# Kernel tuning notes

Hardware: AMD Instinct MI355X
Metric: run time of the kernel (lower is better)

## Reference

```python
import jax, jax.numpy as jnp
import numpy as np

TEMPERATURE = 0.1


def setup_inputs() -> dict:
    key = jax.random.key(0)
    k1, k2 = jax.random.split(key)
    N, D = 4096, 128
    return {
        "anchor_embeddings": jax.random.normal(k1, (N, D), dtype=jnp.float32),
        "target_embeddings": jax.random.normal(k2, (N, D), dtype=jnp.float32),
    }


def _l2_normalize(x, axis=-1, eps=1e-12):
    # matches tf.math.l2_normalize
    sq = jnp.sum(x * x, axis=axis, keepdims=True)
    return x * jax.lax.rsqrt(jnp.maximum(sq, eps))


def reference(anchor_embeddings, target_embeddings):
    N = anchor_embeddings.shape[0]
    # l2-normalize both views; cosine_similarity of unit vectors == dot product,
    # so the original's broadcasted (2N,2N,D) product + internal re-normalization
    # reduces to a single [2N,D] @ [D,2N] matmul.
    a = _l2_normalize(anchor_embeddings, axis=1)
    t = _l2_normalize(target_embeddings, axis=1)
    z = jnp.concatenate([a, t], axis=0)              # [2N, D]
    sim = jnp.einsum("id,jd->ij", z, z)              # [2N, 2N]

    # positives: diag_part(k=+N) and diag_part(k=-N)
    sim_ij = jnp.diagonal(sim, offset=N)             # [N]
    sim_ji = jnp.diagonal(sim, offset=-N)            # [N]
    positives = jnp.concatenate([sim_ij, sim_ji], axis=0)  # [2N]

    logits = sim / TEMPERATURE                       # [2N, 2N]
    # negative_mask = ~eye(2N): exclude self-similarity from the denominator
    diag_mask = jnp.eye(2 * N, dtype=bool)
    denom = jnp.sum(jnp.where(diag_mask, 0.0, jnp.exp(logits)), axis=1)  # [2N]

    loss_partial = -(positives / TEMPERATURE - jnp.log(denom))           # [2N]
    loss = jnp.sum(loss_partial) / (2 * N)
    return loss
```

## Files before the change

kernel.cpp:

```cpp
#include <hip/hip_runtime.h>

#define N_ROWS 4096
#define TN 8192
#define DIM 128
#define SQRT_C 3.79828266f

#define Z_BYTE_OFF 36864

typedef __attribute__((ext_vector_type(8))) short short8;
typedef __attribute__((ext_vector_type(4))) float f32x4;

static __device__ __forceinline__ ushort f2bf(float f) {
    union { float f; unsigned u; } a; a.f = f;
    unsigned r = a.u + 0x7FFF + ((a.u >> 16) & 1);
    return (ushort)(r >> 16);
}

__global__ __launch_bounds__(256) void prep_kernel(
    const float* __restrict__ anchor, const float* __restrict__ target,
    ushort* __restrict__ z, float* __restrict__ pos_part)
{
    int wave = threadIdx.x >> 6;
    int lane = threadIdx.x & 63;
    int i    = blockIdx.x * 4 + wave;
    float2 a = ((const float2*)(anchor + (size_t)i * DIM))[lane];
    float2 t = ((const float2*)(target + (size_t)i * DIM))[lane];
    float sa = a.x * a.x + a.y * a.y;
    float st = t.x * t.x + t.y * t.y;
    float dt = a.x * t.x + a.y * t.y;
    #pragma unroll
    for (int m = 1; m < 64; m <<= 1) {
        sa += __shfl_xor(sa, m, 64);
        st += __shfl_xor(st, m, 64);
        dt += __shfl_xor(dt, m, 64);
    }
    float rsa = rsqrtf(fmaxf(sa, 1e-12f));
    float rst = rsqrtf(fmaxf(st, 1e-12f));
    float ka = rsa * SQRT_C, kt = rst * SQRT_C;
    ushort2 za, zt;
    za.x = f2bf(a.x * ka); za.y = f2bf(a.y * ka);
    zt.x = f2bf(t.x * kt); zt.y = f2bf(t.y * kt);
    ((ushort2*)(z + (size_t)i * DIM))[lane] = za;
    ((ushort2*)(z + (size_t)(i + N_ROWS) * DIM))[lane] = zt;
    __shared__ float red[4];
    if (lane == 0) red[wave] = dt * rsa * rst;
    __syncthreads();
    if (threadIdx.x == 0)
        pos_part[blockIdx.x] = red[0] + red[1] + red[2] + red[3];
}

__global__ __launch_bounds__(256) void simgemm_kernel(
    const ushort* __restrict__ z, float* __restrict__ denom)
{
    int wave = threadIdx.x >> 6;
    int lane = threadIdx.x & 63;
    int r = lane & 15;
    int g = lane >> 4;
    int wr = wave >> 1, wc = wave & 1;
    int rowbase = blockIdx.x * 128 + wr * 64;
    int wcol    = blockIdx.y * 512 + wc * 256;

    short8 a[4][4];
    #pragma unroll
    for (int rt = 0; rt < 4; ++rt)
        #pragma unroll
        for (int kt = 0; kt < 4; ++kt)
            a[rt][kt] = *(const short8*)(z + (size_t)(rowbase + rt * 16 + r) * DIM
                                           + kt * 32 + g * 8);

    float ps[4][4];
    #pragma unroll
    for (int rt = 0; rt < 4; ++rt)
        #pragma unroll
        for (int q = 0; q < 4; ++q) ps[rt][q] = 0.0f;

    bool wavediag = ((unsigned)(rowbase - wcol) < 256u);

    const ushort* pb = z + (size_t)(wcol + r) * DIM + g * 8;

#define LOADB(buf, ptr)                                \
    {   buf[0] = *(const short8*)(ptr);                \
        buf[1] = *(const short8*)((ptr) + 32);         \
        buf[2] = *(const short8*)((ptr) + 64);         \
        buf[3] = *(const short8*)((ptr) + 96); }

#define COMPUTE(ct, b)                                                        \
    {   int c0 = wcol + (ct) * 16;                                            \
        bool dtile = wavediag && ((unsigned)(c0 - rowbase) < 64u);            \
        if (!dtile) {                                                         \
            _Pragma("unroll")                                                 \
            for (int rt = 0; rt < 4; ++rt) {                                  \
                f32x4 acc = {0.f, 0.f, 0.f, 0.f};                             \
                _Pragma("unroll")                                             \
                for (int kt = 0; kt < 4; ++kt)                                \
                    acc = __builtin_amdgcn_mfma_f32_16x16x32_bf16(            \
                        a[rt][kt], b[kt], acc, 0, 0, 0);                      \
                _Pragma("unroll")                                             \
                for (int q = 0; q < 4; ++q)                                   \
                    ps[rt][q] += __builtin_amdgcn_exp2f(acc[q]);              \
            }                                                                 \
        } else {                                                              \
            int gcol = c0 + r;                                                \
            _Pragma("unroll")                                                 \
            for (int rt = 0; rt < 4; ++rt) {                                  \
                f32x4 acc = {0.f, 0.f, 0.f, 0.f};                             \
                _Pragma("unroll")                                             \
                for (int kt = 0; kt < 4; ++kt)                                \
                    acc = __builtin_amdgcn_mfma_f32_16x16x32_bf16(            \
                        a[rt][kt], b[kt], acc, 0, 0, 0);                      \
                _Pragma("unroll")                                             \
                for (int q = 0; q < 4; ++q) {                                 \
                    float e = __builtin_amdgcn_exp2f(acc[q]);                 \
                    int grow = rowbase + rt * 16 + g * 4 + q;                 \
                    ps[rt][q] += (grow == gcol) ? 0.0f : e;                   \
                }                                                             \
            }                                                                 \
        } }

    short8 b0[4], b1[4];
    LOADB(b0, pb);
    for (int ct = 0; ct < 16; ct += 2) {
        const ushort* pn = pb + (ct + 1) * (16 * DIM);
        LOADB(b1, pn);
        COMPUTE(ct, b0);
        if (ct + 2 < 16) {
            const ushort* pn2 = pb + (ct + 2) * (16 * DIM);
            LOADB(b0, pn2);
        }
        COMPUTE(ct + 1, b1);
    }
#undef LOADB
#undef COMPUTE

    #pragma unroll
    for (int rt = 0; rt < 4; ++rt)
        #pragma unroll
        for (int q = 0; q < 4; ++q) {
            float v = ps[rt][q];
            v += __shfl_xor(v, 1, 64);
            v += __shfl_xor(v, 2, 64);
            v += __shfl_xor(v, 4, 64);
            v += __shfl_xor(v, 8, 64);
            if (r == 0)
                atomicAdd(&denom[rowbase + rt * 16 + g * 4 + q], v);
        }
}

__global__ __launch_bounds__(1024) void finalize_kernel(
    const float* __restrict__ denom, const float* __restrict__ pos_part,
    float* __restrict__ out)
{
    int tid = threadIdx.x;
    float slog = 0.0f;
    #pragma unroll
    for (int u = 0; u < TN / 1024; ++u) slog += logf(denom[u * 1024 + tid]);
    float spos = pos_part[tid];
    #pragma unroll
    for (int m = 1; m < 64; m <<= 1) {
        slog += __shfl_xor(slog, m, 64);
        spos += __shfl_xor(spos, m, 64);
    }
    __shared__ float redl[16], redp[16];
    if ((tid & 63) == 0) { redl[tid >> 6] = slog; redp[tid >> 6] = spos; }
    __syncthreads();
    if (tid == 0) {
        float tl = 0.0f, tp = 0.0f;
        #pragma unroll
        for (int i = 0; i < 16; ++i) { tl += redl[i]; tp += redp[i]; }
        out[0] = (tl - 20.0f * tp) / (float)TN;
    }
}

extern "C" void kernel_launch(void* const* d_in, const int* in_sizes, int n_in,
                              void* d_out, int out_size, void* d_ws, size_t ws_size,
                              hipStream_t stream) {
    const float* anchor = (const float*)d_in[0];
    const float* target = (const float*)d_in[1];
    float* denom    = (float*)d_ws;
    float* pos_part = denom + TN;
    ushort* z       = (ushort*)((char*)d_ws + Z_BYTE_OFF);

    hipMemsetAsync(d_ws, 0, TN * sizeof(float), stream);
    prep_kernel<<<N_ROWS / 4, 256, 0, stream>>>(anchor, target, z, pos_part);
    simgemm_kernel<<<dim3(TN / 128, 16), 256, 0, stream>>>(z, denom);
    finalize_kernel<<<1, 1024, 0, stream>>>(denom, pos_part, (float*)d_out);
}
```

Measured before the change: 104.0 us.

## Fuse memset and finalize into neighbouring kernels, retile GEMM with deeper prefetch

The host memset is dropped: prep_kernel now zeroes the denom buffer and the ticket itself. The separate finalize kernel is removed, and the last GEMM block to finish (found through an atomic ticket) computes the final loss. The GEMM tiling is reshaped to 64 rows by 1024 columns per block, and each wave now holds 2 A row tiles, walks 32 column tiles, prefetches three tiles ahead and asks for 2 blocks per CU. This cuts launch overhead and register pressure, at the cost of fewer A rows reused per B load and a serial tail reduction inside a single block.

```diff
diff --git a/kernel.cpp b/kernel.cpp
--- a/kernel.cpp
+++ b/kernel.cpp
@@ -5,7 +5,8 @@
 #define DIM 128
 #define SQRT_C 3.79828266f
 
-#define Z_BYTE_OFF 36864
+#define Z_BYTE_OFF 40960
+#define NBLOCKS_GEMM 1024
 
 typedef __attribute__((ext_vector_type(8))) short short8;
 typedef __attribute__((ext_vector_type(4))) float f32x4;
@@ -18,8 +19,12 @@
 
 __global__ __launch_bounds__(256) void prep_kernel(
     const float* __restrict__ anchor, const float* __restrict__ target,
-    ushort* __restrict__ z, float* __restrict__ pos_part)
+    ushort* __restrict__ z, float* __restrict__ pos_part,
+    float* __restrict__ denom, unsigned* __restrict__ ticket)
 {
+    if (threadIdx.x < 8) denom[blockIdx.x * 8 + threadIdx.x] = 0.0f;
+    if (blockIdx.x == 0 && threadIdx.x == 8) *ticket = 0u;
+
     int wave = threadIdx.x >> 6;
     int lane = threadIdx.x & 63;
     int i    = blockIdx.x * 4 + wave;
@@ -49,47 +54,51 @@
         pos_part[blockIdx.x] = red[0] + red[1] + red[2] + red[3];
 }
 
-__global__ __launch_bounds__(256) void simgemm_kernel(
-    const ushort* __restrict__ z, float* __restrict__ denom)
+__global__ __launch_bounds__(256, 2) void simgemm_kernel(
+    const ushort* __restrict__ z, float* __restrict__ denom,
+    const float* __restrict__ pos_part, unsigned* __restrict__ ticket,
+    float* __restrict__ out)
 {
     int wave = threadIdx.x >> 6;
     int lane = threadIdx.x & 63;
     int r = lane & 15;
     int g = lane >> 4;
     int wr = wave >> 1, wc = wave & 1;
-    int rowbase = blockIdx.x * 128 + wr * 64;
-    int wcol    = blockIdx.y * 512 + wc * 256;
-
-    short8 a[4][4];
-    #pragma unroll
-    for (int rt = 0; rt < 4; ++rt)
-        #pragma unroll
-        for (int kt = 0; kt < 4; ++kt)
+    int rowbase = blockIdx.x * 64 + wr * 32;
+    int wcol    = blockIdx.y * 1024 + wc * 512;
+
+    short8 a[2][4];
+    #pragma unroll
+    for (int rt = 0; rt < 2; ++rt)
+        #pragma unroll
+        for (int kt = 0; kt < 4; ++kt) {
             a[rt][kt] = *(const short8*)(z + (size_t)(rowbase + rt * 16 + r) * DIM
                                            + kt * 32 + g * 8);
-
-    float ps[4][4];
-    #pragma unroll
-    for (int rt = 0; rt < 4; ++rt)
+            asm volatile("" : "+v"(*(f32x4*)&a[rt][kt]));
+        }
+
+    float ps[2][4];
+    #pragma unroll
+    for (int rt = 0; rt < 2; ++rt)
         #pragma unroll
         for (int q = 0; q < 4; ++q) ps[rt][q] = 0.0f;
 
-    bool wavediag = ((unsigned)(rowbase - wcol) < 256u);
-
+    bool wavediag = ((unsigned)(rowbase - wcol) < 512u);
     const ushort* pb = z + (size_t)(wcol + r) * DIM + g * 8;
 
-#define LOADB(buf, ptr)                                \
-    {   buf[0] = *(const short8*)(ptr);                \
-        buf[1] = *(const short8*)((ptr) + 32);         \
-        buf[2] = *(const short8*)((ptr) + 64);         \
-        buf[3] = *(const short8*)((ptr) + 96); }
-
-#define COMPUTE(ct, b)                                                        \
-    {   int c0 = wcol + (ct) * 16;                                            \
-        bool dtile = wavediag && ((unsigned)(c0 - rowbase) < 64u);            \
+#define LOADB(buf, t)                                                  \
+    {   const ushort* p_ = pb + (size_t)(t) * (16 * DIM);              \
+        buf[0] = *(const short8*)(p_);                                 \
+        buf[1] = *(const short8*)(p_ + 32);                            \
+        buf[2] = *(const short8*)(p_ + 64);                            \
+        buf[3] = *(const short8*)(p_ + 96); }
+
+#define COMPUTE(t, b)                                                         \
+    {   int c0 = wcol + (t) * 16;                                             \
+        bool dtile = wavediag && ((unsigned)(c0 - rowbase) < 32u);            \
         if (!dtile) {                                                         \
             _Pragma("unroll")                                                 \
-            for (int rt = 0; rt < 4; ++rt) {                                  \
+            for (int rt = 0; rt < 2; ++rt) {                                  \
                 f32x4 acc = {0.f, 0.f, 0.f, 0.f};                             \
                 _Pragma("unroll")                                             \
                 for (int kt = 0; kt < 4; ++kt)                                \
@@ -102,7 +111,7 @@
         } else {                                                              \
             int gcol = c0 + r;                                                \
             _Pragma("unroll")                                                 \
-            for (int rt = 0; rt < 4; ++rt) {                                  \
+            for (int rt = 0; rt < 2; ++rt) {                                  \
                 f32x4 acc = {0.f, 0.f, 0.f, 0.f};                             \
                 _Pragma("unroll")                                             \
                 for (int kt = 0; kt < 4; ++kt)                                \
@@ -117,23 +126,24 @@
             }                                                                 \
         } }
 
-    short8 b0[4], b1[4];
-    LOADB(b0, pb);
-    for (int ct = 0; ct < 16; ct += 2) {
-        const ushort* pn = pb + (ct + 1) * (16 * DIM);
-        LOADB(b1, pn);
-        COMPUTE(ct, b0);
-        if (ct + 2 < 16) {
-            const ushort* pn2 = pb + (ct + 2) * (16 * DIM);
-            LOADB(b0, pn2);
-        }
-        COMPUTE(ct + 1, b1);
+    short8 b0[4], b1[4], b2[4], b3[4];
+    LOADB(b0, 0); LOADB(b1, 1); LOADB(b2, 2);
+    #pragma unroll
+    for (int t = 0; t < 32; t += 4) {
+        LOADB(b3, t + 3);
+        COMPUTE(t, b0);
+        LOADB(b0, (t + 4 <= 31 ? t + 4 : 31));
+        COMPUTE(t + 1, b1);
+        LOADB(b1, (t + 5 <= 31 ? t + 5 : 31));
+        COMPUTE(t + 2, b2);
+        LOADB(b2, (t + 6 <= 31 ? t + 6 : 31));
+        COMPUTE(t + 3, b3);
     }
 #undef LOADB
 #undef COMPUTE
 
     #pragma unroll
-    for (int rt = 0; rt < 4; ++rt)
+    for (int rt = 0; rt < 2; ++rt)
         #pragma unroll
         for (int q = 0; q < 4; ++q) {
             float v = ps[rt][q];
@@ -144,30 +154,40 @@
             if (r == 0)
                 atomicAdd(&denom[rowbase + rt * 16 + g * 4 + q], v);
         }
-}
-
-__global__ __launch_bounds__(1024) void finalize_kernel(
-    const float* __restrict__ denom, const float* __restrict__ pos_part,
-    float* __restrict__ out)
-{
-    int tid = threadIdx.x;
-    float slog = 0.0f;
-    #pragma unroll
-    for (int u = 0; u < TN / 1024; ++u) slog += logf(denom[u * 1024 + tid]);
-    float spos = pos_part[tid];
-    #pragma unroll
-    for (int m = 1; m < 64; m <<= 1) {
-        slog += __shfl_xor(slog, m, 64);
-        spos += __shfl_xor(spos, m, 64);
-    }
-    __shared__ float redl[16], redp[16];
-    if ((tid & 63) == 0) { redl[tid >> 6] = slog; redp[tid >> 6] = spos; }
+
     __syncthreads();
-    if (tid == 0) {
-        float tl = 0.0f, tp = 0.0f;
-        #pragma unroll
-        for (int i = 0; i < 16; ++i) { tl += redl[i]; tp += redp[i]; }
-        out[0] = (tl - 20.0f * tp) / (float)TN;
+    __shared__ int islast;
+    if (threadIdx.x == 0) {
+        __threadfence();
+        islast = (atomicAdd(ticket, 1u) == NBLOCKS_GEMM - 1) ? 1 : 0;
+    }
+    __syncthreads();
+    if (islast) {
+        int tid = threadIdx.x;
+        float slog = 0.0f;
+        #pragma unroll
+        for (int u = 0; u < TN / 256; ++u) {
+            float d = __hip_atomic_load(&denom[u * 256 + tid],
+                                        __ATOMIC_RELAXED, __HIP_MEMORY_SCOPE_AGENT);
+            slog += logf(d);
+        }
+        float spos = 0.0f;
+        #pragma unroll
+        for (int u = 0; u < 1024 / 256; ++u)
+            spos += pos_part[u * 256 + tid];
+        #pragma unroll
+        for (int m = 1; m < 64; m <<= 1) {
+            slog += __shfl_xor(slog, m, 64);
+            spos += __shfl_xor(spos, m, 64);
+        }
+        __shared__ float redl[4], redp[4];
+        if ((tid & 63) == 0) { redl[tid >> 6] = slog; redp[tid >> 6] = spos; }
+        __syncthreads();
+        if (tid == 0) {
+            float tl = redl[0] + redl[1] + redl[2] + redl[3];
+            float tp = redp[0] + redp[1] + redp[2] + redp[3];
+            out[0] = (tl - 20.0f * tp) / (float)TN;
+        }
     }
 }
 
@@ -176,12 +196,13 @@
                               hipStream_t stream) {
     const float* anchor = (const float*)d_in[0];
     const float* target = (const float*)d_in[1];
-    float* denom    = (float*)d_ws;
-    float* pos_part = denom + TN;
-    ushort* z       = (ushort*)((char*)d_ws + Z_BYTE_OFF);
-
-    hipMemsetAsync(d_ws, 0, TN * sizeof(float), stream);
-    prep_kernel<<<N_ROWS / 4, 256, 0, stream>>>(anchor, target, z, pos_part);
-    simgemm_kernel<<<dim3(TN / 128, 16), 256, 0, stream>>>(z, denom);
-    finalize_kernel<<<1, 1024, 0, stream>>>(denom, pos_part, (float*)d_out);
-}
+    float* denom       = (float*)d_ws;
+    float* pos_part    = denom + TN;
+    unsigned* ticket   = (unsigned*)(pos_part + 1024);
+    ushort* z          = (ushort*)((char*)d_ws + Z_BYTE_OFF);
+
+    prep_kernel<<<N_ROWS / 4, 256, 0, stream>>>(anchor, target, z, pos_part,
+                                                denom, ticket);
+    simgemm_kernel<<<dim3(TN / 64, TN / 1024), 256, 0, stream>>>(
+        z, denom, pos_part, ticket, (float*)d_out);
+}
```

Measured after the change: 196.8 us. +89.2%, slower.
